# Optimization experiments

Measured on AMD Instinct MI355X. Metric: run time of the kernel, lower is better.

## Reference

```python
import jax, jax.numpy as jnp
import numpy as np

B, H_TRAJ, S = 8, 16, 64
DIM, C = 128, 2000
D = 2 * DIM            # transformer d_model
NUM_HEADS, WINDOW, L = 4, 4, 2
D_FF = 4 * D


def setup_inputs() -> dict:
    key = jax.random.key(0)
    ks = jax.random.split(key, 12)
    w = lambda k, shape, s: jax.random.normal(k, shape, jnp.float32) * s
    return {
        "history": jax.random.randint(ks[0], (B, H_TRAJ, S), 0, C + 1),
        "current_trajectory": jax.random.randint(ks[1], (B, S), 0, C + 1),
        "embedding": w(ks[2], (1, C, DIM), 1.0),
        "null_embedding": jax.random.uniform(ks[3], (D,), jnp.float32),
        "gcn_w": w(ks[4], (DIM, DIM), 0.05),
        "gcn_b": jnp.zeros((DIM,), jnp.float32),
        "enc_attn_w": w(ks[5], (L, 4, D, D), 0.05),
        "enc_attn_b": jnp.zeros((L, 4, D), jnp.float32),
        "enc_ffn_w1": w(ks[6], (L, D, D_FF), 0.05),
        "enc_ffn_b1": jnp.zeros((L, D_FF), jnp.float32),
        "enc_ffn_w2": w(ks[7], (L, D_FF, D), 0.05),
        "enc_ffn_b2": jnp.zeros((L, D), jnp.float32),
        "enc_ln_s": jnp.ones((L, 2, D), jnp.float32),
        "enc_ln_b": jnp.zeros((L, 2, D), jnp.float32),
        "wca_w": w(ks[8], (4, D, D), 0.05),
        "wca_b": jnp.zeros((4, D), jnp.float32),
        "ial_w": w(ks[9], (D, DIM), 0.05),
        "ial_b": jnp.zeros((DIM,), jnp.float32),
    }


def _layer_norm(x, s, b, eps=1e-5):
    m = x.mean(-1, keepdims=True)
    v = ((x - m) ** 2).mean(-1, keepdims=True)
    return (x - m) * jax.lax.rsqrt(v + eps) * s + b


def _mha(xq, xkv, w, b, mask):
    # w: (4,d,d) q/k/v/out, b: (4,d); mask additive, broadcast over heads
    d = xq.shape[-1]
    hd = d // NUM_HEADS
    proj = lambda x, i: (x @ w[i] + b[i]).reshape(x.shape[:-1] + (NUM_HEADS, hd))
    q, k, v = proj(xq, 0), proj(xkv, 1), proj(xkv, 2)
    s = jnp.einsum('bqhd,bkhd->bhqk', q, k) / float(np.sqrt(hd))
    s = s + mask[:, None, :, :]
    a = jax.nn.softmax(s, axis=-1)
    o = jnp.einsum('bhqk,bkhd->bqhd', a, v).reshape(xq.shape)
    return o @ w[3] + b[3]


def _get_graph(history):
    # vectorized scatter-add replacement of the python triple loop
    src, dst = history[:, :, :-1], history[:, :, 1:]
    h_idx = jnp.arange(H_TRAJ, dtype=jnp.float32)
    wts = 1.0 + jnp.exp(-0.01 * (H_TRAJ - 1 - h_idx))          # per-trajectory weight
    valid = (src != C) & (dst != C) & (src != dst)
    wv = jnp.where(valid, wts[None, :, None], 0.0)
    sc, dc = jnp.clip(src, 0, C - 1), jnp.clip(dst, 0, C - 1)
    flat = (jnp.arange(B)[:, None, None] * C * C + sc * C + dc).ravel()
    A = jnp.zeros((B * C * C,), jnp.float32).at[flat].add(wv.ravel())
    return A.reshape(B, C, C)


def _mytransform(A):
    A = A + jnp.eye(C, dtype=A.dtype)
    d = jnp.sqrt(A.sum(axis=1))          # torch code: sqrt of dim-1 sums (no inverse)
    return d[:, :, None] * A * d[:, None, :]   # D @ A @ D


def _temporal(seq_len, d):
    t = jnp.arange(seq_len, dtype=jnp.float32)[:, None]
    den = 10000.0 ** (jnp.arange(0, d, 2, dtype=jnp.float32) / d)
    arg = t / den[None, :]
    return jnp.stack([jnp.sin(arg), jnp.cos(arg)], axis=-1).reshape(seq_len, d)


def _fuse(pos, hist, temp, null_emb):
    # pos: (B,C,D); hist: (B,...,S); gather + where fusion
    g = jax.vmap(lambda p, h: p[h])(pos, jnp.clip(hist, 0, C - 1))
    return jnp.where((hist == C)[..., None], null_emb + temp, g + temp)


def _encoder(x, mask, aw, ab, fw1, fb1, fw2, fb2, lns, lnb):
    for l in range(L):
        a = _mha(x, x, aw[l], ab[l], mask)
        x = _layer_norm(x + a, lns[l, 0], lnb[l, 0])
        f = jax.nn.relu(x @ fw1[l] + fb1[l]) @ fw2[l] + fb2[l]
        x = _layer_norm(x + f, lns[l, 1], lnb[l, 1])
    return x


def reference(history, current_trajectory, embedding, null_embedding, gcn_w, gcn_b,
              enc_attn_w, enc_attn_b, enc_ffn_w1, enc_ffn_b1, enc_ffn_w2, enc_ffn_b2,
              enc_ln_s, enc_ln_b, wca_w, wca_b, ial_w, ial_b):
    E = jnp.broadcast_to(embedding, (B, C, DIM))
    A = _mytransform(_get_graph(history))                      # (B,C,C)
    Eg = jax.nn.relu(A @ E @ gcn_w + gcn_b)                    # GCN layer
    pos = jnp.concatenate([E, Eg], axis=-1)                    # (B,C,2*dim)
    temp = _temporal(S, D)
    fh = _fuse(pos, history, temp, null_embedding).reshape(B * H_TRAJ, S, D)
    fc = _fuse(pos, current_trajectory, temp, null_embedding)  # (B,S,D)
    hmask = jnp.broadcast_to(
        jnp.where((history == C)[:, :, None, :], -jnp.inf, 0.0),
        (B, H_TRAJ, S, S)).reshape(B * H_TRAJ, S, S)
    cmask = jnp.broadcast_to(
        jnp.where((current_trajectory == C)[:, None, :], -jnp.inf, 0.0), (B, S, S))
    mh = _encoder(fh, hmask, enc_attn_w, enc_attn_b, enc_ffn_w1, enc_ffn_b1,
                  enc_ffn_w2, enc_ffn_b2, enc_ln_s, enc_ln_b)
    mc = _encoder(fc, cmask, enc_attn_w, enc_attn_b, enc_ffn_w1, enc_ffn_b1,
                  enc_ffn_w2, enc_ffn_b2, enc_ln_s, enc_ln_b)
    cur_rep = jnp.broadcast_to(mc[:, None], (B, H_TRAJ, S, D)).reshape(B * H_TRAJ, S, D)
    i = jnp.arange(S)
    wmask = jnp.where(jnp.abs(i[:, None] - i[None, :]) <= WINDOW, 0.0, -jnp.inf)[None]
    wca = mh + _mha(mh, cur_rep, wca_w, wca_b, wmask)          # window-based cross attn
    wca = wca.reshape(B, H_TRAJ, S, D)
    # information aggregation over the trajectory axis
    scores = jnp.einsum('bhsd,bsd->bhs', wca, mc) / float(np.sqrt(D))
    aw = jax.nn.softmax(scores, axis=1)
    agg = jnp.einsum('bhs,bhsd->bsd', aw, wca)
    final = jax.nn.relu((agg + mc) @ ial_w + ial_b)            # (B,S,dim)
    return final @ embedding[0].T                              # (B,S,C)
```

## Files before the change

kernel.cpp:

```cpp
#include <hip/hip_runtime.h>
#include <hip/hip_bf16.h>
#include <math.h>

#define C_N   2000
#define DIMN  128
#define DM    256
#define B_N   8
#define HT    16
#define S_N   64
#define NSEQ  136
#define DFF   1024
#define NEDGE (B_N*HT*(S_N-1))

typedef __hip_bfloat16 bf16;
typedef short bf16x8 __attribute__((ext_vector_type(8)));
typedef float f32x4  __attribute__((ext_vector_type(4)));

#define GLOAD_LDS16(gp, lp) \
    __builtin_amdgcn_global_load_lds((const __attribute__((address_space(1))) void*)(gp), \
                                     (__attribute__((address_space(3))) void*)(lp), 16, 0, 0)

__device__ __forceinline__ short f2bf(float v) {
    bf16 t = (bf16)v;
    return *reinterpret_cast<short*>(&t);
}


__global__ void k_initX(const float* __restrict__ cs, const float* __restrict__ Y,
                        const float* __restrict__ gb, float* __restrict__ Eg) {
    size_t i = (size_t)blockIdx.x * 256 + threadIdx.x;
    int k = (int)(i % DIMN); size_t bc = i / DIMN;
    int c = (int)(bc % C_N); int b = (int)(bc / C_N);
    float dd2 = 1.f + cs[b * C_N + c];
    Eg[i] = dd2 * Y[(size_t)c * DIMN + k] + gb[k];
}

__global__ void k_edgeX(const int* __restrict__ hist, const float* __restrict__ cs,
                        const float* __restrict__ Y, float* __restrict__ Eg) {
    int e = blockIdx.x;
    int s = e % (S_N-1); int bh = e / (S_N-1); int h = bh % HT; int b = bh / HT;
    const int* row = hist + (size_t)bh * S_N;
    int src = row[s], dst = row[s+1];
    if (src == C_N || dst == C_N || src == dst) return;
    float w = (1.f + expf(-0.01f * (float)(HT - 1 - h)))
            * sqrtf(1.f + cs[b*C_N+src]) * sqrtf(1.f + cs[b*C_N+dst]);
    int k = threadIdx.x;
    atomicAdd(&Eg[((size_t)b * C_N + src) * DIMN + k], w * Y[(size_t)dst * DIMN + k]);
}

struct TEnt { const float* s; bf16* d; int K; int N; int nm; int tiles; };
struct PrepArgs {
    TEnt e[6];
    const float* emb; bf16* embbf;
    const int* hist; float* colsum;
    float* temp;
};

__global__ void k_prep(PrepArgs p) {
    int id = blockIdx.x;
    int t = threadIdx.y * 32 + threadIdx.x;
    if (id < 1840) {
        __shared__ float tl[32][33];
        TEnt en = p.e[0];
        #pragma unroll
        for (int k = 0; k < 6; ++k) {
            if (id < p.e[k].tiles) { en = p.e[k]; break; }
            id -= p.e[k].tiles;
        }
        int tn = en.N >> 5;
        int per = (en.K >> 5) * tn;
        int mat = id / per, t2 = id % per;
        int ty = t2 / tn, tx = t2 % tn;
        const float* s = en.s + (size_t)mat * en.K * en.N;
        bf16* d = en.d + (size_t)mat * en.N * en.K;
        int k0 = ty * 32, n0 = tx * 32;
        #pragma unroll
        for (int j = 0; j < 32; j += 8)
            tl[threadIdx.y + j][threadIdx.x] = s[(size_t)(k0 + threadIdx.y + j) * en.N + n0 + threadIdx.x];
        __syncthreads();
        #pragma unroll
        for (int j = 0; j < 32; j += 8)
            d[(size_t)(n0 + threadIdx.y + j) * en.K + k0 + threadIdx.x] = (bf16)tl[threadIdx.x][threadIdx.y + j];
        return;
    }
    id -= 1840;
    if (id < 250) {
        int i = (id * 256 + t) * 4;
        float4 v = *(const float4*)(p.emb + i);
        bf16* d = p.embbf;
        d[i] = (bf16)v.x; d[i+1] = (bf16)v.y; d[i+2] = (bf16)v.z; d[i+3] = (bf16)v.w;
        return;
    }
    id -= 250;
    if (id < 32) {
        int e = id * 256 + t;
        if (e >= NEDGE) return;
        int s = e % (S_N-1); int bh = e / (S_N-1); int h = bh % HT; int b = bh / HT;
        const int* row = p.hist + (size_t)bh * S_N;
        int src = row[s], dst = row[s+1];
        if (src != C_N && dst != C_N && src != dst) {
            float w = 1.f + expf(-0.01f * (float)(HT - 1 - h));
            atomicAdd(&p.colsum[b * C_N + dst], w);
        }
        return;
    }
    id -= 32;
    {
        int s = id; int d = t;
        int k = d >> 1;
        float den = powf(10000.f, (2.f * (float)k) / 256.f);
        float arg = (float)s / den;
        p.temp[s * DM + d] = (d & 1) ? cosf(arg) : sinf(arg);
    }
}

template<int EPI>
__global__ __launch_bounds__(256) void k_bgemm(
        const bf16* __restrict__ A, const bf16* __restrict__ Bt,
        const float* __restrict__ bias, const float* __restrict__ resid,
        void* __restrict__ Cout, int M, int N, int K, int ldc, int nreal)
{
    __shared__ bf16 As[2][128 * 64];
    __shared__ bf16 Bs[2][64 * 64];
    int tid = threadIdx.x;
    int wid = tid >> 6, lane = tid & 63;
    int m0 = blockIdx.y * 128, n0 = blockIdx.x * 64;
    int wr = wid >> 1, wc = wid & 1;
    int lr = lane >> 3, lc = lane & 7;
    int gc = lc ^ lr;
    f32x4 acc[4][2] = {};
    int nkt = K >> 6;

#define STAGE_BG(kt, buf) { \
    int kb = (kt) << 6; \
    _Pragma("unroll") \
    for (int s = 0; s < 4; ++s) { \
        int seg = wid * 4 + s; int row = seg * 8 + lr; \
        GLOAD_LDS16(A + (size_t)(m0 + row) * K + kb + gc * 8, &As[buf][seg * 512]); \
    } \
    _Pragma("unroll") \
    for (int s = 0; s < 2; ++s) { \
        int seg = wid * 2 + s; int row = seg * 8 + lr; \
        GLOAD_LDS16(Bt + (size_t)(n0 + row) * K + kb + gc * 8, &Bs[buf][seg * 512]); \
    } }

    STAGE_BG(0, 0);
    __syncthreads();
    int cur = 0;
    for (int kt = 0; kt < nkt; ++kt) {
        if (kt + 1 < nkt) STAGE_BG(kt + 1, cur ^ 1);
        #pragma unroll
        for (int kk = 0; kk < 2; ++kk) {
            bf16x8 af[4], bfr[2];
            int c = kk * 4 + (lane >> 4);
            #pragma unroll
            for (int m = 0; m < 4; ++m) {
                int row = wr * 64 + m * 16 + (lane & 15);
                af[m] = *(const bf16x8*)(&As[cur][row * 64 + (c ^ (row & 7)) * 8]);
            }
            #pragma unroll
            for (int n = 0; n < 2; ++n) {
                int row = wc * 32 + n * 16 + (lane & 15);
                bfr[n] = *(const bf16x8*)(&Bs[cur][row * 64 + (c ^ (row & 7)) * 8]);
            }
            #pragma unroll
            for (int m = 0; m < 4; ++m)
                #pragma unroll
                for (int n = 0; n < 2; ++n)
                    acc[m][n] = __builtin_amdgcn_mfma_f32_16x16x32_bf16(af[m], bfr[n], acc[m][n], 0, 0, 0);
        }
        __syncthreads();
        cur ^= 1;
    }
#undef STAGE_BG
    int cl = lane & 15, ch = lane >> 4;
    #pragma unroll
    for (int n = 0; n < 2; ++n) {
        int col = n0 + wc * 32 + n * 16 + cl;
        if ((EPI & 16) && col >= nreal) continue;
        float bv = (EPI & 1) ? bias[col] : 0.f;
        #pragma unroll
        for (int m = 0; m < 4; ++m) {
            #pragma unroll
            for (int j = 0; j < 4; ++j) {
                int row = m0 + wr * 64 + m * 16 + ch * 4 + j;
                float v = acc[m][n][j] + bv;
                if (EPI & 4) v += resid[(size_t)row * ldc + col];
                if (EPI & 2) v = fmaxf(v, 0.f);
                if (EPI & 8) ((bf16*)Cout)[(size_t)row * ldc + col] = (bf16)v;
                else         ((float*)Cout)[(size_t)row * ldc + col] = v;
            }
        }
    }
}

__global__ __launch_bounds__(256) void k_bgemm_ln(
        const bf16* __restrict__ A, const bf16* __restrict__ Bt,
        const float* __restrict__ bias, float* __restrict__ Xf,
        const float* __restrict__ lns_, const float* __restrict__ lnb_,
        bf16* __restrict__ Xb, int M, int K)
{
    __shared__ bf16 As[2][32 * 64];
    __shared__ bf16 Bs[2][256 * 64];
    __shared__ float ls1[32][4], ls2[32][4];
    int tid = threadIdx.x, wid = tid >> 6, lane = tid & 63;
    int lr = lane >> 3, lc = lane & 7, gc = lc ^ lr;
    int cl = lane & 15, ch = lane >> 4;
    int m0 = blockIdx.x * 32;
    int wc = wid;
    f32x4 acc[2][4] = {};
    int nkt = K >> 6;

#define STAGE_LN(kt, buf) { \
    int kb = (kt) << 6; \
    { int row = wid * 8 + lr; \
      GLOAD_LDS16(A + (size_t)(m0 + row) * K + kb + gc * 8, &As[buf][wid * 512]); } \
    _Pragma("unroll") \
    for (int s = 0; s < 8; ++s) { \
        int seg = wid * 8 + s; int row = seg * 8 + lr; \
        GLOAD_LDS16(Bt + (size_t)row * K + kb + gc * 8, &Bs[buf][seg * 512]); \
    } }

    STAGE_LN(0, 0);
    __syncthreads();
    int cur = 0;
    for (int kt = 0; kt < nkt; ++kt) {
        if (kt + 1 < nkt) STAGE_LN(kt + 1, cur ^ 1);
        #pragma unroll
        for (int kk = 0; kk < 2; ++kk) {
            int c = kk * 4 + ch;
            bf16x8 af[2], bfr[4];
            #pragma unroll
            for (int m = 0; m < 2; ++m) {
                int row = m * 16 + cl;
                af[m] = *(const bf16x8*)(&As[cur][row * 64 + (c ^ (row & 7)) * 8]);
            }
            #pragma unroll
            for (int n = 0; n < 4; ++n) {
                int row = wc * 64 + n * 16 + cl;
                bfr[n] = *(const bf16x8*)(&Bs[cur][row * 64 + (c ^ (row & 7)) * 8]);
            }
            #pragma unroll
            for (int m = 0; m < 2; ++m)
                #pragma unroll
                for (int n = 0; n < 4; ++n)
                    acc[m][n] = __builtin_amdgcn_mfma_f32_16x16x32_bf16(af[m], bfr[n], acc[m][n], 0, 0, 0);
        }
        __syncthreads();
        cur ^= 1;
    }
#undef STAGE_LN
    #pragma unroll
    for (int m = 0; m < 2; ++m) {
        #pragma unroll
        for (int j = 0; j < 4; ++j) {
            int rl = m * 16 + ch * 4 + j;
            float s1 = 0.f, s2 = 0.f;
            #pragma unroll
            for (int n = 0; n < 4; ++n) {
                int col = wc * 64 + n * 16 + cl;
                float v = acc[m][n][j] + bias[col] + Xf[(size_t)(m0 + rl) * 256 + col];
                acc[m][n][j] = v;
                s1 += v; s2 += v * v;
            }
            s1 += __shfl_xor(s1, 1); s2 += __shfl_xor(s2, 1);
            s1 += __shfl_xor(s1, 2); s2 += __shfl_xor(s2, 2);
            s1 += __shfl_xor(s1, 4); s2 += __shfl_xor(s2, 4);
            s1 += __shfl_xor(s1, 8); s2 += __shfl_xor(s2, 8);
            if (cl == 0) { ls1[rl][wc] = s1; ls2[rl][wc] = s2; }
        }
    }
    __syncthreads();
    #pragma unroll
    for (int m = 0; m < 2; ++m) {
        #pragma unroll
        for (int j = 0; j < 4; ++j) {
            int rl = m * 16 + ch * 4 + j;
            float su = ls1[rl][0] + ls1[rl][1] + ls1[rl][2] + ls1[rl][3];
            float sq = ls2[rl][0] + ls2[rl][1] + ls2[rl][2] + ls2[rl][3];
            float mean = su * (1.f / 256.f);
            float var  = sq * (1.f / 256.f) - mean * mean;
            float rstd = rsqrtf(var + 1e-5f);
            #pragma unroll
            for (int n = 0; n < 4; ++n) {
                int col = wc * 64 + n * 16 + cl;
                float r = (acc[m][n][j] - mean) * rstd * lns_[col] + lnb_[col];
                size_t g = (size_t)(m0 + rl) * 256 + col;
                Xf[g] = r;
                Xb[g] = (bf16)r;
            }
        }
    }
}


__global__ void k_fuse(const int* __restrict__ hist, const int* __restrict__ cur,
                       const float* __restrict__ E, const float* __restrict__ Eg,
                       const float* __restrict__ nullE, const float* __restrict__ temp,
                       float* __restrict__ Xenc, bf16* __restrict__ Xbf,
                       float* __restrict__ maskb) {
    int blk = blockIdx.x;
    int seq = blk >> 6, s = blk & 63;
    int d = threadIdx.x;
    int idx, b;
    if (seq < 128) { b = seq >> 4; idx = hist[(size_t)seq * S_N + s]; }
    else           { b = seq - 128; idx = cur[b * S_N + s]; }
    float t = temp[s * DM + d];
    float v;
    if (idx == C_N) v = nullE[d] + t;
    else {
        v = ((d < DIMN) ? E[(size_t)idx * DIMN + d]
                        : fmaxf(Eg[((size_t)b * C_N + idx) * DIMN + (d - DIMN)], 0.f)) + t;
    }
    size_t o = ((size_t)seq * S_N + s) * DM + d;
    Xenc[o] = v;
    Xbf[o]  = (bf16)v;
    if (d == 0) maskb[seq * S_N + s] = (idx == C_N) ? -INFINITY : 0.f;
}

template<bool WCA>
__global__ __launch_bounds__(64) void k_mattn(
        const bf16* __restrict__ Qb, const bf16* __restrict__ Kb,
        const bf16* __restrict__ Vb, const float* __restrict__ maskb,
        bf16* __restrict__ O, int qstr, int kstr)
{
    int seq = blockIdx.x >> 2, head = blockIdx.x & 3;
    int lane = threadIdx.x;
    int cl = lane & 15, ch = lane >> 4;
    __shared__ __align__(16) short VT[64 * 72];
    __shared__ __align__(16) short PT[64 * 72];

    const bf16* Qp = Qb + (size_t)seq * 64 * qstr + head * 64;
    int kvseq = WCA ? (seq >> 4) : seq;
    const bf16* Kp = Kb + (size_t)kvseq * 64 * kstr + head * 64;
    const bf16* Vp = Vb + (size_t)kvseq * 64 * kstr + head * 64;

    bf16x8 aq[4][2], bk[4][2], vr[4][2];
    #pragma unroll
    for (int t = 0; t < 4; ++t)
        #pragma unroll
        for (int kk = 0; kk < 2; ++kk) {
            int row = t * 16 + cl, d0 = kk * 32 + ch * 8;
            aq[t][kk] = *(const bf16x8*)(Qp + (size_t)row * qstr + d0);
            bk[t][kk] = *(const bf16x8*)(Kp + (size_t)row * kstr + d0);
            vr[t][kk] = *(const bf16x8*)(Vp + (size_t)row * kstr + d0);
        }

    f32x4 sa[4][4] = {};
    #pragma unroll
    for (int kk = 0; kk < 2; ++kk)
        #pragma unroll
        for (int m = 0; m < 4; ++m)
            #pragma unroll
            for (int n = 0; n < 4; ++n)
                sa[m][n] = __builtin_amdgcn_mfma_f32_16x16x32_bf16(aq[m][kk], bk[n][kk], sa[m][n], 0, 0, 0);

    #pragma unroll
    for (int t = 0; t < 4; ++t)
        #pragma unroll
        for (int kk = 0; kk < 2; ++kk) {
            int k = t * 16 + cl, d0 = kk * 32 + ch * 8;
            #pragma unroll
            for (int e = 0; e < 8; ++e)
                VT[(d0 + e) * 72 + k] = vr[t][kk][e];
        }

    float mk4[4];
    if (!WCA) {
        #pragma unroll
        for (int n = 0; n < 4; ++n) mk4[n] = maskb[seq * 64 + n * 16 + cl];
    }

    #pragma unroll
    for (int m = 0; m < 4; ++m) {
        #pragma unroll
        for (int j = 0; j < 4; ++j) {
            int q = m * 16 + ch * 4 + j;
            float rm = -INFINITY;
            #pragma unroll
            for (int n = 0; n < 4; ++n) {
                int k = n * 16 + cl;
                float msk = WCA ? ((abs(q - k) <= 4) ? 0.f : -INFINITY) : mk4[n];
                float v = sa[m][n][j] * 0.125f + msk;
                sa[m][n][j] = v;
                rm = fmaxf(rm, v);
            }
            rm = fmaxf(rm, __shfl_xor(rm, 1));
            rm = fmaxf(rm, __shfl_xor(rm, 2));
            rm = fmaxf(rm, __shfl_xor(rm, 4));
            rm = fmaxf(rm, __shfl_xor(rm, 8));
            float rs = 0.f;
            #pragma unroll
            for (int n = 0; n < 4; ++n) {
                float e = expf(sa[m][n][j] - rm);
                sa[m][n][j] = e;
                rs += e;
            }
            rs += __shfl_xor(rs, 1);
            rs += __shfl_xor(rs, 2);
            rs += __shfl_xor(rs, 4);
            rs += __shfl_xor(rs, 8);
            float inv = 1.f / rs;
            #pragma unroll
            for (int n = 0; n < 4; ++n)
                PT[q * 72 + n * 16 + cl] = f2bf(sa[m][n][j] * inv);
        }
    }
    __syncthreads();

    f32x4 oa[4][4] = {};
    #pragma unroll
    for (int kk = 0; kk < 2; ++kk) {
        bf16x8 av[4], bp[4];
        #pragma unroll
        for (int dm = 0; dm < 4; ++dm)
            av[dm] = *(const bf16x8*)(VT + (dm * 16 + cl) * 72 + kk * 32 + ch * 8);
        #pragma unroll
        for (int qn = 0; qn < 4; ++qn)
            bp[qn] = *(const bf16x8*)(PT + (qn * 16 + cl) * 72 + kk * 32 + ch * 8);
        #pragma unroll
        for (int dm = 0; dm < 4; ++dm)
            #pragma unroll
            for (int qn = 0; qn < 4; ++qn)
                oa[dm][qn] = __builtin_amdgcn_mfma_f32_16x16x32_bf16(av[dm], bp[qn], oa[dm][qn], 0, 0, 0);
    }
    __syncthreads();

    #pragma unroll
    for (int dm = 0; dm < 4; ++dm)
        #pragma unroll
        for (int qn = 0; qn < 4; ++qn)
            #pragma unroll
            for (int j = 0; j < 4; ++j)
                PT[(qn * 16 + cl) * 72 + dm * 16 + ch * 4 + j] = f2bf(oa[dm][qn][j]);
    __syncthreads();
    #pragma unroll
    for (int it = 0; it < 8; ++it) {
        int chunk = it * 64 + lane;
        int tok = chunk >> 3, d0 = (chunk & 7) * 8;
        bf16x8 v = *(const bf16x8*)(PT + tok * 72 + d0);
        *(bf16x8*)(O + ((size_t)seq * 64 + tok) * 256 + head * 64 + d0) = v;
    }
}


__global__ __launch_bounds__(256) void k_agg(const float* __restrict__ wca,
                                             const float* __restrict__ mc,
                                             bf16* __restrict__ aggbf) {
    int bs = blockIdx.x; int b = bs >> 6, s = bs & 63;
    int d = threadIdx.x;
    __shared__ float red[4][16];
    float mcv = mc[((size_t)b * S_N + s) * DM + d];
    float wv[16], p[16];
    #pragma unroll
    for (int h = 0; h < 16; ++h) {
        wv[h] = wca[(((size_t)(b * HT + h)) * S_N + s) * DM + d];
        p[h] = wv[h] * mcv;
    }
    #pragma unroll
    for (int o = 1; o < 64; o <<= 1)
        #pragma unroll
        for (int h = 0; h < 16; ++h) p[h] += __shfl_xor(p[h], o);
    if ((d & 63) == 0) {
        int w = d >> 6;
        #pragma unroll
        for (int h = 0; h < 16; ++h) red[w][h] = p[h];
    }
    __syncthreads();
    float sc[16], mx = -INFINITY;
    #pragma unroll
    for (int h = 0; h < 16; ++h) {
        sc[h] = (red[0][h] + red[1][h] + red[2][h] + red[3][h]) * (1.f / 16.f);
        mx = fmaxf(mx, sc[h]);
    }
    float e[16], sum = 0.f;
    #pragma unroll
    for (int h = 0; h < 16; ++h) { e[h] = expf(sc[h] - mx); sum += e[h]; }
    float inv = 1.f / sum;
    float acc = 0.f;
    #pragma unroll
    for (int h = 0; h < 16; ++h) acc += e[h] * inv * wv[h];
    aggbf[((size_t)b * S_N + s) * DM + d] = (bf16)(acc + mcv);
}


extern "C" void kernel_launch(void* const* d_in, const int* in_sizes, int n_in,
                              void* d_out, int out_size, void* d_ws, size_t ws_size,
                              hipStream_t stream) {
    const int*   history = (const int*)d_in[0];
    const int*   cur     = (const int*)d_in[1];
    const float* emb     = (const float*)d_in[2];
    const float* nullE   = (const float*)d_in[3];
    const float* gcn_w   = (const float*)d_in[4];
    const float* gcn_b   = (const float*)d_in[5];
    const float* aw      = (const float*)d_in[6];
    const float* ab      = (const float*)d_in[7];
    const float* fw1     = (const float*)d_in[8];
    const float* fb1     = (const float*)d_in[9];
    const float* fw2     = (const float*)d_in[10];
    const float* fb2     = (const float*)d_in[11];
    const float* lns     = (const float*)d_in[12];
    const float* lnb     = (const float*)d_in[13];
    const float* wca_w   = (const float*)d_in[14];
    const float* wca_b   = (const float*)d_in[15];
    const float* ial_w   = (const float*)d_in[16];
    const float* ial_b   = (const float*)d_in[17];
    float* out = (float*)d_out;
    float* ws  = (float*)d_ws;

    float* dvec   = ws + 0;
    float* maskb  = ws + 16000;
    float* temp   = ws + 24704;
    bf16*  aggbf  = (bf16*)(ws + 41088);
    bf16*  finalb = (bf16*)(ws + 106624);
    bf16*  embbf  = (bf16*)(ws + 139392);
    float* Y      = ws + 270464;
    float* Eg     = ws + 532608;
    bf16*  wbf    = (bf16*)(ws + 2580608);
    float* Xenc   = ws + 3522688;
    bf16*  Xbf    = (bf16*)(ws + 5750912);
    bf16*  Abf    = (bf16*)(ws + 6865024);
    bf16*  Hbf    = (bf16*)(ws + 7979136);
    bf16*  QKVbf  = (bf16*)(ws + 12435584);
    float* SE     = ws + 15777920;

    bf16* wbf_aw  = wbf;
    bf16* wbf_fw1 = wbf + 524288;
    bf16* wbf_fw2 = wbf + 1048576;
    bf16* wbf_wca = wbf + 1572864;
    bf16* wbf_gcn = wbf + 1835008;
    bf16* wbf_ial = wbf + 1851392;

    bf16* Qwbf = QKVbf;
    bf16* KVbf = QKVbf + 4194304;

    hipMemsetAsync(dvec, 0, 16000 * sizeof(float), stream);
    hipMemsetAsync(embbf + 2000 * 128, 0, 48 * 128 * sizeof(bf16), stream);
    PrepArgs pa;
    pa.e[0] = { aw,    wbf_aw,  256,  256, 8, 512 };
    pa.e[1] = { fw1,   wbf_fw1, 256, 1024, 2, 512 };
    pa.e[2] = { fw2,   wbf_fw2, 1024, 256, 2, 512 };
    pa.e[3] = { wca_w, wbf_wca, 256,  256, 4, 256 };
    pa.e[4] = { gcn_w, wbf_gcn, 128,  128, 1,  16 };
    pa.e[5] = { ial_w, wbf_ial, 256,  128, 1,  32 };
    pa.emb = emb; pa.embbf = embbf;
    pa.hist = history; pa.colsum = dvec;
    pa.temp = temp;
    k_prep<<<1840 + 250 + 32 + 64, dim3(32, 8), 0, stream>>>(pa);

    k_bgemm<0><<<dim3(2, 16), 256, 0, stream>>>(embbf, wbf_gcn, nullptr, nullptr, Y,
                                                2048, DIMN, DIMN, DIMN, DIMN);
    k_initX<<<B_N * C_N * DIMN / 256, 256, 0, stream>>>(dvec, Y, gcn_b, Eg);
    k_edgeX<<<NEDGE, 128, 0, stream>>>(history, dvec, Y, Eg);

    k_fuse<<<NSEQ * S_N, DM, 0, stream>>>(history, cur, emb, Eg, nullE, temp, Xenc, Xbf, maskb);

    for (int l = 0; l < 2; ++l) {
        k_bgemm<9><<<dim3(12, 68), 256, 0, stream>>>(Xbf, wbf_aw + l * 262144,
                ab + l * 1024, nullptr, QKVbf, NSEQ * S_N, 768, 256, 768, 768);
        k_mattn<false><<<NSEQ * 4, 64, 0, stream>>>(QKVbf, QKVbf + 256, QKVbf + 512,
                maskb, Abf, 768, 768);
        k_bgemm_ln<<<272, 256, 0, stream>>>(Abf, wbf_aw + l * 262144 + 196608,
                ab + l * 1024 + 768, Xenc, lns + (l * 2 + 0) * DM, lnb + (l * 2 + 0) * DM,
                Xbf, NSEQ * S_N, 256);
        k_bgemm<11><<<dim3(16, 68), 256, 0, stream>>>(Xbf, wbf_fw1 + l * 262144,
                fb1 + l * DFF, nullptr, Hbf, NSEQ * S_N, DFF, 256, DFF, DFF);
        k_bgemm_ln<<<272, 256, 0, stream>>>(Hbf, wbf_fw2 + l * 262144,
                fb2 + l * DM, Xenc, lns + (l * 2 + 1) * DM, lnb + (l * 2 + 1) * DM,
                Xbf, NSEQ * S_N, 1024);
    }

    float* mh = Xenc;
    bf16*  mc_bf = Xbf + (size_t)128 * S_N * DM;

    k_bgemm<9><<<dim3(4, 64), 256, 0, stream>>>(Xbf, wbf_wca, wca_b, nullptr, Qwbf,
                                                128 * S_N, 256, 256, 256, 256);
    k_bgemm<9><<<dim3(8, 4), 256, 0, stream>>>(mc_bf, wbf_wca + 65536, wca_b + 256, nullptr,
                                               KVbf, B_N * S_N, 512, 256, 512, 512);
    k_mattn<true><<<128 * 4, 64, 0, stream>>>(Qwbf, KVbf, KVbf + 256, nullptr, Abf, 256, 512);
    k_bgemm<5><<<dim3(4, 64), 256, 0, stream>>>(Abf, wbf_wca + 196608, wca_b + 768, mh, SE,
                                                128 * S_N, 256, 256, 256, 256);

    k_agg<<<B_N * S_N, 256, 0, stream>>>(SE, Xenc + (size_t)128 * S_N * DM, aggbf);
    k_bgemm<11><<<dim3(2, 4), 256, 0, stream>>>(aggbf, wbf_ial, ial_b, nullptr, finalb,
                                                B_N * S_N, DIMN, DM, DIMN, DIMN);
    k_bgemm<16><<<dim3(32, 4), 256, 0, stream>>>(finalb, embbf, nullptr, nullptr, out,
                                                 B_N * S_N, 2048, DIMN, C_N, C_N);
}
```

Before: 320.7 us.

## Fuse whole pipeline into one cooperative persistent megakernel with grid syncs

```diff
diff --git a/kernel.cpp b/kernel.cpp
--- a/kernel.cpp
+++ b/kernel.cpp
@@ -1,4 +1,5 @@
 #include <hip/hip_runtime.h>
+#include <hip/hip_cooperative_groups.h>
 #include <hip/hip_bf16.h>
 #include <math.h>
 
@@ -16,6 +17,8 @@
 typedef short bf16x8 __attribute__((ext_vector_type(8)));
 typedef float f32x4  __attribute__((ext_vector_type(4)));
 
+namespace cg = cooperative_groups;
+
 #define GLOAD_LDS16(gp, lp) \
     __builtin_amdgcn_global_load_lds((const __attribute__((address_space(1))) void*)(gp), \
                                      (__attribute__((address_space(3))) void*)(lp), 16, 0, 0)
@@ -25,158 +28,98 @@
     return *reinterpret_cast<short*>(&t);
 }
 
-
-__global__ void k_initX(const float* __restrict__ cs, const float* __restrict__ Y,
-                        const float* __restrict__ gb, float* __restrict__ Eg) {
-    size_t i = (size_t)blockIdx.x * 256 + threadIdx.x;
-    int k = (int)(i % DIMN); size_t bc = i / DIMN;
-    int c = (int)(bc % C_N); int b = (int)(bc / C_N);
-    float dd2 = 1.f + cs[b * C_N + c];
-    Eg[i] = dd2 * Y[(size_t)c * DIMN + k] + gb[k];
-}
-
-__global__ void k_edgeX(const int* __restrict__ hist, const float* __restrict__ cs,
-                        const float* __restrict__ Y, float* __restrict__ Eg) {
-    int e = blockIdx.x;
-    int s = e % (S_N-1); int bh = e / (S_N-1); int h = bh % HT; int b = bh / HT;
-    const int* row = hist + (size_t)bh * S_N;
-    int src = row[s], dst = row[s+1];
-    if (src == C_N || dst == C_N || src == dst) return;
-    float w = (1.f + expf(-0.01f * (float)(HT - 1 - h)))
-            * sqrtf(1.f + cs[b*C_N+src]) * sqrtf(1.f + cs[b*C_N+dst]);
-    int k = threadIdx.x;
-    atomicAdd(&Eg[((size_t)b * C_N + src) * DIMN + k], w * Y[(size_t)dst * DIMN + k]);
-}
-
-struct TEnt { const float* s; bf16* d; int K; int N; int nm; int tiles; };
-struct PrepArgs {
-    TEnt e[6];
-    const float* emb; bf16* embbf;
-    const int* hist; float* colsum;
-    float* temp;
+struct MegaArgs {
+    const int *hist, *cur;
+    const float *emb, *nullE, *gcn_b, *ab, *fb1, *fb2, *lns, *lnb, *wca_b, *ial_b;
+    const float *w_aw, *w_fw1, *w_fw2, *w_wca, *w_gcn, *w_ial;
+    float *dvec, *maskb, *temp, *Y, *Eg, *Xenc, *SE, *out;
+    bf16 *embbf, *wbf_aw, *wbf_fw1, *wbf_fw2, *wbf_wca, *wbf_gcn, *wbf_ial;
+    bf16 *Xbf, *Abf, *Hbf, *QKV, *finalb;
 };
 
-__global__ void k_prep(PrepArgs p) {
-    int id = blockIdx.x;
-    int t = threadIdx.y * 32 + threadIdx.x;
-    if (id < 1840) {
-        __shared__ float tl[32][33];
-        TEnt en = p.e[0];
-        #pragma unroll
-        for (int k = 0; k < 6; ++k) {
-            if (id < p.e[k].tiles) { en = p.e[k]; break; }
-            id -= p.e[k].tiles;
-        }
-        int tn = en.N >> 5;
-        int per = (en.K >> 5) * tn;
-        int mat = id / per, t2 = id % per;
-        int ty = t2 / tn, tx = t2 % tn;
-        const float* s = en.s + (size_t)mat * en.K * en.N;
-        bf16* d = en.d + (size_t)mat * en.N * en.K;
-        int k0 = ty * 32, n0 = tx * 32;
-        #pragma unroll
-        for (int j = 0; j < 32; j += 8)
-            tl[threadIdx.y + j][threadIdx.x] = s[(size_t)(k0 + threadIdx.y + j) * en.N + n0 + threadIdx.x];
-        __syncthreads();
-        #pragma unroll
-        for (int j = 0; j < 32; j += 8)
-            d[(size_t)(n0 + threadIdx.y + j) * en.K + k0 + threadIdx.x] = (bf16)tl[threadIdx.x][threadIdx.y + j];
-        return;
-    }
-    id -= 1840;
-    if (id < 250) {
-        int i = (id * 256 + t) * 4;
-        float4 v = *(const float4*)(p.emb + i);
-        bf16* d = p.embbf;
-        d[i] = (bf16)v.x; d[i+1] = (bf16)v.y; d[i+2] = (bf16)v.z; d[i+3] = (bf16)v.w;
-        return;
-    }
-    id -= 250;
-    if (id < 32) {
-        int e = id * 256 + t;
-        if (e >= NEDGE) return;
-        int s = e % (S_N-1); int bh = e / (S_N-1); int h = bh % HT; int b = bh / HT;
-        const int* row = p.hist + (size_t)bh * S_N;
-        int src = row[s], dst = row[s+1];
-        if (src != C_N && dst != C_N && src != dst) {
-            float w = 1.f + expf(-0.01f * (float)(HT - 1 - h));
-            atomicAdd(&p.colsum[b * C_N + dst], w);
-        }
-        return;
-    }
-    id -= 32;
-    {
-        int s = id; int d = t;
-        int k = d >> 1;
-        float den = powf(10000.f, (2.f * (float)k) / 256.f);
-        float arg = (float)s / den;
-        p.temp[s * DM + d] = (d & 1) ? cosf(arg) : sinf(arg);
-    }
+
+__device__ __forceinline__ void transp_unit(const float* __restrict__ src, bf16* __restrict__ dst,
+                                            int K, int N, int tileid, float (*tl)[33]) {
+    int tx = threadIdx.x & 31, ty = (threadIdx.x >> 5) & 7;
+    int tn = N >> 5;
+    int per = (K >> 5) * tn;
+    int mat = tileid / per, t2 = tileid % per;
+    int tyy = t2 / tn, txx = t2 % tn;
+    const float* s = src + (size_t)mat * K * N;
+    bf16* d = dst + (size_t)mat * N * K;
+    int k0 = tyy * 32, n0 = txx * 32;
+    #pragma unroll
+    for (int j = 0; j < 32; j += 8)
+        tl[ty + j][tx] = s[(size_t)(k0 + ty + j) * N + n0 + tx];
+    __syncthreads();
+    #pragma unroll
+    for (int j = 0; j < 32; j += 8)
+        d[(size_t)(n0 + ty + j) * K + k0 + tx] = (bf16)tl[tx][ty + j];
+    __syncthreads();
 }
 
 template<int EPI>
-__global__ __launch_bounds__(256) void k_bgemm(
+__device__ __forceinline__ void bgemm2_tile(
         const bf16* __restrict__ A, const bf16* __restrict__ Bt,
         const float* __restrict__ bias, const float* __restrict__ resid,
-        void* __restrict__ Cout, int M, int N, int K, int ldc, int nreal)
+        void* __restrict__ Cout, int m0, int n0, int K, int ldc, int nreal, char* smemc)
 {
-    __shared__ bf16 As[2][128 * 64];
-    __shared__ bf16 Bs[2][64 * 64];
+    bf16* As = (bf16*)smemc;
+    bf16* Bs = (bf16*)(smemc + 32768);
     int tid = threadIdx.x;
     int wid = tid >> 6, lane = tid & 63;
-    int m0 = blockIdx.y * 128, n0 = blockIdx.x * 64;
     int wr = wid >> 1, wc = wid & 1;
     int lr = lane >> 3, lc = lane & 7;
     int gc = lc ^ lr;
-    f32x4 acc[4][2] = {};
+    f32x4 acc[4][4] = {};
     int nkt = K >> 6;
 
-#define STAGE_BG(kt, buf) { \
+#define STAGE2(kt, buf) { \
     int kb = (kt) << 6; \
     _Pragma("unroll") \
     for (int s = 0; s < 4; ++s) { \
         int seg = wid * 4 + s; int row = seg * 8 + lr; \
-        GLOAD_LDS16(A + (size_t)(m0 + row) * K + kb + gc * 8, &As[buf][seg * 512]); \
+        GLOAD_LDS16(A + (size_t)(m0 + row) * K + kb + gc * 8, As + (buf) * 8192 + seg * 512); \
     } \
     _Pragma("unroll") \
-    for (int s = 0; s < 2; ++s) { \
-        int seg = wid * 2 + s; int row = seg * 8 + lr; \
-        GLOAD_LDS16(Bt + (size_t)(n0 + row) * K + kb + gc * 8, &Bs[buf][seg * 512]); \
+    for (int s = 0; s < 4; ++s) { \
+        int seg = wid * 4 + s; int row = seg * 8 + lr; \
+        GLOAD_LDS16(Bt + (size_t)(n0 + row) * K + kb + gc * 8, Bs + (buf) * 8192 + seg * 512); \
     } }
 
-    STAGE_BG(0, 0);
+    STAGE2(0, 0);
     __syncthreads();
     int cur = 0;
     for (int kt = 0; kt < nkt; ++kt) {
-        if (kt + 1 < nkt) STAGE_BG(kt + 1, cur ^ 1);
+        if (kt + 1 < nkt) STAGE2(kt + 1, cur ^ 1);
         #pragma unroll
         for (int kk = 0; kk < 2; ++kk) {
-            bf16x8 af[4], bfr[2];
+            bf16x8 af[4], bfr[4];
             int c = kk * 4 + (lane >> 4);
             #pragma unroll
             for (int m = 0; m < 4; ++m) {
                 int row = wr * 64 + m * 16 + (lane & 15);
-                af[m] = *(const bf16x8*)(&As[cur][row * 64 + (c ^ (row & 7)) * 8]);
-            }
-            #pragma unroll
-            for (int n = 0; n < 2; ++n) {
-                int row = wc * 32 + n * 16 + (lane & 15);
-                bfr[n] = *(const bf16x8*)(&Bs[cur][row * 64 + (c ^ (row & 7)) * 8]);
+                af[m] = *(const bf16x8*)(As + cur * 8192 + row * 64 + (c ^ (row & 7)) * 8);
+            }
+            #pragma unroll
+            for (int n = 0; n < 4; ++n) {
+                int row = wc * 64 + n * 16 + (lane & 15);
+                bfr[n] = *(const bf16x8*)(Bs + cur * 8192 + row * 64 + (c ^ (row & 7)) * 8);
             }
             #pragma unroll
             for (int m = 0; m < 4; ++m)
                 #pragma unroll
-                for (int n = 0; n < 2; ++n)
+                for (int n = 0; n < 4; ++n)
                     acc[m][n] = __builtin_amdgcn_mfma_f32_16x16x32_bf16(af[m], bfr[n], acc[m][n], 0, 0, 0);
         }
         __syncthreads();
         cur ^= 1;
     }
-#undef STAGE_BG
+#undef STAGE2
     int cl = lane & 15, ch = lane >> 4;
     #pragma unroll
-    for (int n = 0; n < 2; ++n) {
-        int col = n0 + wc * 32 + n * 16 + cl;
+    for (int n = 0; n < 4; ++n) {
+        int col = n0 + wc * 64 + n * 16 + cl;
         if ((EPI & 16) && col >= nreal) continue;
         float bv = (EPI & 1) ? bias[col] : 0.f;
         #pragma unroll
@@ -194,19 +137,19 @@
     }
 }
 
-__global__ __launch_bounds__(256) void k_bgemm_ln(
+__device__ __forceinline__ void bgemm_ln_tile(
         const bf16* __restrict__ A, const bf16* __restrict__ Bt,
         const float* __restrict__ bias, float* __restrict__ Xf,
         const float* __restrict__ lns_, const float* __restrict__ lnb_,
-        bf16* __restrict__ Xb, int M, int K)
+        bf16* __restrict__ Xb, int m0, int K, char* smemc)
 {
-    __shared__ bf16 As[2][32 * 64];
-    __shared__ bf16 Bs[2][256 * 64];
-    __shared__ float ls1[32][4], ls2[32][4];
+    bf16* As  = (bf16*)smemc;
+    bf16* Bs  = (bf16*)(smemc + 8192);
+    float* ls1 = (float*)(smemc + 73728);
+    float* ls2 = ls1 + 128;
     int tid = threadIdx.x, wid = tid >> 6, lane = tid & 63;
     int lr = lane >> 3, lc = lane & 7, gc = lc ^ lr;
     int cl = lane & 15, ch = lane >> 4;
-    int m0 = blockIdx.x * 32;
     int wc = wid;
     f32x4 acc[2][4] = {};
     int nkt = K >> 6;
@@ -214,11 +157,11 @@
 #define STAGE_LN(kt, buf) { \
     int kb = (kt) << 6; \
     { int row = wid * 8 + lr; \
-      GLOAD_LDS16(A + (size_t)(m0 + row) * K + kb + gc * 8, &As[buf][wid * 512]); } \
+      GLOAD_LDS16(A + (size_t)(m0 + row) * K + kb + gc * 8, As + (buf) * 2048 + wid * 512); } \
     _Pragma("unroll") \
     for (int s = 0; s < 8; ++s) { \
         int seg = wid * 8 + s; int row = seg * 8 + lr; \
-        GLOAD_LDS16(Bt + (size_t)row * K + kb + gc * 8, &Bs[buf][seg * 512]); \
+        GLOAD_LDS16(Bt + (size_t)row * K + kb + gc * 8, Bs + (buf) * 16384 + seg * 512); \
     } }
 
     STAGE_LN(0, 0);
@@ -233,12 +176,12 @@
             #pragma unroll
             for (int m = 0; m < 2; ++m) {
                 int row = m * 16 + cl;
-                af[m] = *(const bf16x8*)(&As[cur][row * 64 + (c ^ (row & 7)) * 8]);
+                af[m] = *(const bf16x8*)(As + cur * 2048 + row * 64 + (c ^ (row & 7)) * 8);
             }
             #pragma unroll
             for (int n = 0; n < 4; ++n) {
                 int row = wc * 64 + n * 16 + cl;
-                bfr[n] = *(const bf16x8*)(&Bs[cur][row * 64 + (c ^ (row & 7)) * 8]);
+                bfr[n] = *(const bf16x8*)(Bs + cur * 16384 + row * 64 + (c ^ (row & 7)) * 8);
             }
             #pragma unroll
             for (int m = 0; m < 2; ++m)
@@ -267,7 +210,7 @@
             s1 += __shfl_xor(s1, 2); s2 += __shfl_xor(s2, 2);
             s1 += __shfl_xor(s1, 4); s2 += __shfl_xor(s2, 4);
             s1 += __shfl_xor(s1, 8); s2 += __shfl_xor(s2, 8);
-            if (cl == 0) { ls1[rl][wc] = s1; ls2[rl][wc] = s2; }
+            if (cl == 0) { ls1[rl * 4 + wc] = s1; ls2[rl * 4 + wc] = s2; }
         }
     }
     __syncthreads();
@@ -276,8 +219,8 @@
         #pragma unroll
         for (int j = 0; j < 4; ++j) {
             int rl = m * 16 + ch * 4 + j;
-            float su = ls1[rl][0] + ls1[rl][1] + ls1[rl][2] + ls1[rl][3];
-            float sq = ls2[rl][0] + ls2[rl][1] + ls2[rl][2] + ls2[rl][3];
+            float su = ls1[rl*4+0] + ls1[rl*4+1] + ls1[rl*4+2] + ls1[rl*4+3];
+            float sq = ls2[rl*4+0] + ls2[rl*4+1] + ls2[rl*4+2] + ls2[rl*4+3];
             float mean = su * (1.f / 256.f);
             float var  = sq * (1.f / 256.f) - mean * mean;
             float rstd = rsqrtf(var + 1e-5f);
@@ -291,45 +234,18 @@
             }
         }
     }
-}
-
-
-__global__ void k_fuse(const int* __restrict__ hist, const int* __restrict__ cur,
-                       const float* __restrict__ E, const float* __restrict__ Eg,
-                       const float* __restrict__ nullE, const float* __restrict__ temp,
-                       float* __restrict__ Xenc, bf16* __restrict__ Xbf,
-                       float* __restrict__ maskb) {
-    int blk = blockIdx.x;
-    int seq = blk >> 6, s = blk & 63;
-    int d = threadIdx.x;
-    int idx, b;
-    if (seq < 128) { b = seq >> 4; idx = hist[(size_t)seq * S_N + s]; }
-    else           { b = seq - 128; idx = cur[b * S_N + s]; }
-    float t = temp[s * DM + d];
-    float v;
-    if (idx == C_N) v = nullE[d] + t;
-    else {
-        v = ((d < DIMN) ? E[(size_t)idx * DIMN + d]
-                        : fmaxf(Eg[((size_t)b * C_N + idx) * DIMN + (d - DIMN)], 0.f)) + t;
-    }
-    size_t o = ((size_t)seq * S_N + s) * DM + d;
-    Xenc[o] = v;
-    Xbf[o]  = (bf16)v;
-    if (d == 0) maskb[seq * S_N + s] = (idx == C_N) ? -INFINITY : 0.f;
+    __syncthreads();
 }
 
 template<bool WCA>
-__global__ __launch_bounds__(64) void k_mattn(
-        const bf16* __restrict__ Qb, const bf16* __restrict__ Kb,
+__device__ __forceinline__ void mattn_unit(
+        int seq, int head, const bf16* __restrict__ Qb, const bf16* __restrict__ Kb,
         const bf16* __restrict__ Vb, const float* __restrict__ maskb,
-        bf16* __restrict__ O, int qstr, int kstr)
+        bf16* __restrict__ O, short* VT, short* PT, int lane)
 {
-    int seq = blockIdx.x >> 2, head = blockIdx.x & 3;
-    int lane = threadIdx.x;
+    const int qstr = WCA ? 256 : 768;
+    const int kstr = WCA ? 512 : 768;
     int cl = lane & 15, ch = lane >> 4;
-    __shared__ __align__(16) short VT[64 * 72];
-    __shared__ __align__(16) short PT[64 * 72];
-
     const bf16* Qp = Qb + (size_t)seq * 64 * qstr + head * 64;
     int kvseq = WCA ? (seq >> 4) : seq;
     const bf16* Kp = Kb + (size_t)kvseq * 64 * kstr + head * 64;
@@ -345,7 +261,6 @@
             bk[t][kk] = *(const bf16x8*)(Kp + (size_t)row * kstr + d0);
             vr[t][kk] = *(const bf16x8*)(Vp + (size_t)row * kstr + d0);
         }
-
     f32x4 sa[4][4] = {};
     #pragma unroll
     for (int kk = 0; kk < 2; ++kk)
@@ -354,7 +269,6 @@
             #pragma unroll
             for (int n = 0; n < 4; ++n)
                 sa[m][n] = __builtin_amdgcn_mfma_f32_16x16x32_bf16(aq[m][kk], bk[n][kk], sa[m][n], 0, 0, 0);
-
     #pragma unroll
     for (int t = 0; t < 4; ++t)
         #pragma unroll
@@ -364,13 +278,11 @@
             for (int e = 0; e < 8; ++e)
                 VT[(d0 + e) * 72 + k] = vr[t][kk][e];
         }
-
     float mk4[4];
     if (!WCA) {
         #pragma unroll
         for (int n = 0; n < 4; ++n) mk4[n] = maskb[seq * 64 + n * 16 + cl];
     }
-
     #pragma unroll
     for (int m = 0; m < 4; ++m) {
         #pragma unroll
@@ -407,7 +319,6 @@
         }
     }
     __syncthreads();
-
     f32x4 oa[4][4] = {};
     #pragma unroll
     for (int kk = 0; kk < 2; ++kk) {
@@ -425,7 +336,6 @@
                 oa[dm][qn] = __builtin_amdgcn_mfma_f32_16x16x32_bf16(av[dm], bp[qn], oa[dm][qn], 0, 0, 0);
     }
     __syncthreads();
-
     #pragma unroll
     for (int dm = 0; dm < 4; ++dm)
         #pragma unroll
@@ -443,18 +353,70 @@
     }
 }
 
-
-__global__ __launch_bounds__(256) void k_agg(const float* __restrict__ wca,
-                                             const float* __restrict__ mc,
-                                             bf16* __restrict__ aggbf) {
-    int bs = blockIdx.x; int b = bs >> 6, s = bs & 63;
+__device__ __forceinline__ void fuse_unit(const MegaArgs& a, int u, int d) {
+    int seq = u >> 6, s = u & 63;
+    int idx, b;
+    if (seq < 128) { b = seq >> 4; idx = a.hist[(size_t)seq * S_N + s]; }
+    else           { b = seq - 128; idx = a.cur[b * S_N + s]; }
+    float t = a.temp[s * DM + d];
+    float v;
+    if (idx == C_N) v = a.nullE[d] + t;
+    else {
+        v = ((d < DIMN) ? a.emb[(size_t)idx * DIMN + d]
+                        : fmaxf(a.Eg[((size_t)b * C_N + idx) * DIMN + (d - DIMN)], 0.f)) + t;
+    }
+    size_t o = (size_t)u * DM + d;
+    a.Xenc[o] = v;
+    a.Xbf[o]  = (bf16)v;
+    if (d == 0) a.maskb[u] = (idx == C_N) ? -INFINITY : 0.f;
+}
+
+__device__ __forceinline__ void initx_unit(const MegaArgs& a, int u, int tid) {
+    int i0 = u * 1024 + tid * 4;
+    int k = i0 & 127; int bc = i0 >> 7; int c = bc % C_N; int b = bc / C_N;
+    float dd2 = 1.f + a.dvec[b * C_N + c];
+    float4 y = *(const float4*)(a.Y + (size_t)c * DIMN + k);
+    float4 o = { dd2 * y.x + a.gcn_b[k],     dd2 * y.y + a.gcn_b[k + 1],
+                 dd2 * y.z + a.gcn_b[k + 2], dd2 * y.w + a.gcn_b[k + 3] };
+    *(float4*)(a.Eg + i0) = o;
+}
+
+__device__ __forceinline__ void edge_unit(const MegaArgs& a, int u, int tid) {
+    int e = u * 2 + (tid >> 7); int k = tid & 127;
+    int s = e % (S_N-1); int bh = e / (S_N-1); int h = bh % HT; int b = bh / HT;
+    const int* row = a.hist + (size_t)bh * S_N;
+    int src = row[s], dst = row[s+1];
+    if (src == C_N || dst == C_N || src == dst) return;
+    float w = (1.f + expf(-0.01f * (float)(HT - 1 - h)))
+            * sqrtf(1.f + a.dvec[b*C_N+src]) * sqrtf(1.f + a.dvec[b*C_N+dst]);
+    atomicAdd(&a.Eg[((size_t)b * C_N + src) * DIMN + k], w * a.Y[(size_t)dst * DIMN + k]);
+}
+
+__device__ __forceinline__ void colsum_unit(const MegaArgs& a, int u, int tid) {
+    int e = u * 256 + tid;
+    if (e >= NEDGE) return;
+    int s = e % (S_N-1); int bh = e / (S_N-1); int h = bh % HT; int b = bh / HT;
+    const int* row = a.hist + (size_t)bh * S_N;
+    int src = row[s], dst = row[s+1];
+    if (src != C_N && dst != C_N && src != dst) {
+        float w = 1.f + expf(-0.01f * (float)(HT - 1 - h));
+        atomicAdd(&a.dvec[b * C_N + dst], w);
+    }
+}
+
+__device__ __forceinline__ void agg_ial_unit(int u, const float* __restrict__ SE,
+        const float* __restrict__ mc, const bf16* __restrict__ ialw,
+        const float* __restrict__ ialb, bf16* __restrict__ finalb, char* smemc)
+{
+    float* red  = (float*)smemc;
+    float* aggs = (float*)(smemc + 256);
+    int b = u >> 6, s = u & 63;
     int d = threadIdx.x;
-    __shared__ float red[4][16];
     float mcv = mc[((size_t)b * S_N + s) * DM + d];
     float wv[16], p[16];
     #pragma unroll
     for (int h = 0; h < 16; ++h) {
-        wv[h] = wca[(((size_t)(b * HT + h)) * S_N + s) * DM + d];
+        wv[h] = SE[(((size_t)(b * HT + h)) * S_N + s) * DM + d];
         p[h] = wv[h] * mcv;
     }
     #pragma unroll
@@ -464,13 +426,13 @@
     if ((d & 63) == 0) {
         int w = d >> 6;
         #pragma unroll
-        for (int h = 0; h < 16; ++h) red[w][h] = p[h];
+        for (int h = 0; h < 16; ++h) red[w * 16 + h] = p[h];
     }
     __syncthreads();
     float sc[16], mx = -INFINITY;
     #pragma unroll
     for (int h = 0; h < 16; ++h) {
-        sc[h] = (red[0][h] + red[1][h] + red[2][h] + red[3][h]) * (1.f / 16.f);
+        sc[h] = (red[h] + red[16 + h] + red[32 + h] + red[48 + h]) * (1.f / 16.f);
         mx = fmaxf(mx, sc[h]);
     }
     float e[16], sum = 0.f;
@@ -480,38 +442,184 @@
     float acc = 0.f;
     #pragma unroll
     for (int h = 0; h < 16; ++h) acc += e[h] * inv * wv[h];
-    aggbf[((size_t)b * S_N + s) * DM + d] = (bf16)(acc + mcv);
+    aggs[d] = acc + mcv;
+    __syncthreads();
+    if (d < 128) {
+        float sumo = ialb[d];
+        #pragma unroll 8
+        for (int k = 0; k < 256; ++k) sumo += aggs[k] * (float)ialw[d * 256 + k];
+        finalb[(size_t)u * 128 + d] = (bf16)fmaxf(sumo, 0.f);
+    }
+    __syncthreads();
+}
+
+__device__ __forceinline__ void prep_unit(const MegaArgs& a, int u, int tid, char* smemc) {
+    if (u < 1840) {
+        const float* s; bf16* d; int K, N, t0;
+        if      (u < 512)  { s = a.w_aw;  d = a.wbf_aw;  K = 256;  N = 256;  t0 = u; }
+        else if (u < 1024) { s = a.w_fw1; d = a.wbf_fw1; K = 256;  N = 1024; t0 = u - 512; }
+        else if (u < 1536) { s = a.w_fw2; d = a.wbf_fw2; K = 1024; N = 256;  t0 = u - 1024; }
+        else if (u < 1792) { s = a.w_wca; d = a.wbf_wca; K = 256;  N = 256;  t0 = u - 1536; }
+        else if (u < 1808) { s = a.w_gcn; d = a.wbf_gcn; K = 128;  N = 128;  t0 = u - 1792; }
+        else               { s = a.w_ial; d = a.wbf_ial; K = 256;  N = 128;  t0 = u - 1808; }
+        transp_unit(s, d, K, N, t0, (float(*)[33])smemc);
+    } else if (u < 2090) {
+        int i = ((u - 1840) * 256 + tid) * 4;
+        float4 v = *(const float4*)(a.emb + i);
+        a.embbf[i] = (bf16)v.x; a.embbf[i+1] = (bf16)v.y;
+        a.embbf[i+2] = (bf16)v.z; a.embbf[i+3] = (bf16)v.w;
+    } else if (u < 2154) {
+        int s = u - 2090; int d = tid;
+        int k = d >> 1;
+        float den = powf(10000.f, (2.f * (float)k) / 256.f);
+        float arg = (float)s / den;
+        a.temp[s * DM + d] = (d & 1) ? cosf(arg) : sinf(arg);
+    } else if (u < 2170) {
+        int i4 = (u - 2154) * 256 + tid;
+        if (i4 < 4000) { float4 z = {0,0,0,0}; *(float4*)(a.dvec + i4 * 4) = z; }
+    } else {
+        int* p = (int*)(a.embbf + 2000 * 128);
+        for (int j = tid; j < 3072; j += 256) p[j] = 0;
+    }
+}
+
+
+__global__ __launch_bounds__(256, 2) void k_mega(MegaArgs a) {
+    cg::grid_group grid = cg::this_grid();
+    __shared__ __align__(16) char smem[74752];
+    const int nb = gridDim.x, bid = blockIdx.x;
+    const int tid = threadIdx.x, wid = tid >> 6, lane = tid & 63;
+
+    for (int u = bid; u < 2171; u += nb) prep_unit(a, u, tid, smem);
+    grid.sync();
+    for (int u = bid; u < 48; u += nb) {
+        if (u < 16) bgemm2_tile<0>(a.embbf, a.wbf_gcn, nullptr, nullptr, a.Y,
+                                   u * 128, 0, 128, 128, 0, smem);
+        else colsum_unit(a, u - 16, tid);
+    }
+    grid.sync();
+    for (int u = bid; u < 2000; u += nb) initx_unit(a, u, tid);
+    grid.sync();
+    for (int u = bid; u < 4032; u += nb) edge_unit(a, u, tid);
+    grid.sync();
+    for (int u = bid; u < 8704; u += nb) fuse_unit(a, u, tid);
+    grid.sync();
+    for (int l = 0; l < 2; ++l) {
+        const bf16* wqkv = a.wbf_aw + l * 262144;
+        const float* bl = a.ab + l * 1024;
+        for (int u = bid; u < 408; u += nb)
+            bgemm2_tile<9>(a.Xbf, wqkv, bl, nullptr, a.QKV,
+                           (u / 6) * 128, (u % 6) * 128, 256, 768, 0, smem);
+        grid.sync();
+        for (int u = bid; u < 136; u += nb)
+            mattn_unit<false>(u, wid, a.QKV, a.QKV + 256, a.QKV + 512, a.maskb, a.Abf,
+                              (short*)(smem + wid * 18432), (short*)(smem + wid * 18432 + 9216), lane);
+        grid.sync();
+        for (int u = bid; u < 272; u += nb)
+            bgemm_ln_tile(a.Abf, wqkv + 196608, bl + 768, a.Xenc,
+                          a.lns + (l * 2) * DM, a.lnb + (l * 2) * DM, a.Xbf, u * 32, 256, smem);
+        grid.sync();
+        for (int u = bid; u < 544; u += nb)
+            bgemm2_tile<11>(a.Xbf, a.wbf_fw1 + l * 262144, a.fb1 + l * DFF, nullptr, a.Hbf,
+                            (u / 8) * 128, (u % 8) * 128, 256, DFF, 0, smem);
+        grid.sync();
+        for (int u = bid; u < 272; u += nb)
+            bgemm_ln_tile(a.Hbf, a.wbf_fw2 + l * 262144, a.fb2 + l * DM, a.Xenc,
+                          a.lns + (l * 2 + 1) * DM, a.lnb + (l * 2 + 1) * DM, a.Xbf, u * 32, 1024, smem);
+        grid.sync();
+    }
+    for (int u = bid; u < 144; u += nb) {
+        if (u < 128)
+            bgemm2_tile<9>(a.Xbf, a.wbf_wca, a.wca_b, nullptr, a.QKV,
+                           (u >> 1) * 128, (u & 1) * 128, 256, 256, 0, smem);
+        else {
+            int v = u - 128;
+            bgemm2_tile<9>(a.Xbf + (size_t)128 * S_N * DM, a.wbf_wca + 65536, a.wca_b + 256,
+                           nullptr, a.QKV + 4194304, (v >> 2) * 128, (v & 3) * 128, 256, 512, 0, smem);
+        }
+    }
+    grid.sync();
+    for (int u = bid; u < 128; u += nb)
+        mattn_unit<true>(u, wid, a.QKV, a.QKV + 4194304, a.QKV + 4194304 + 256, nullptr, a.Abf,
+                         (short*)(smem + wid * 18432), (short*)(smem + wid * 18432 + 9216), lane);
+    grid.sync();
+    for (int u = bid; u < 128; u += nb)
+        bgemm2_tile<5>(a.Abf, a.wbf_wca + 196608, a.wca_b + 768, a.Xenc, a.SE,
+                       (u >> 1) * 128, (u & 1) * 128, 256, 256, 0, smem);
+    grid.sync();
+    for (int u = bid; u < 512; u += nb)
+        agg_ial_unit(u, a.SE, a.Xenc + (size_t)128 * S_N * DM, a.wbf_ial, a.ial_b, a.finalb, smem);
+    grid.sync();
+    for (int u = bid; u < 64; u += nb)
+        bgemm2_tile<16>(a.finalb, a.embbf, nullptr, nullptr, a.out,
+                        (u >> 4) * 128, (u & 15) * 128, 128, C_N, C_N, smem);
+}
+
+
+__global__ void k_prepg(MegaArgs a) {
+    __shared__ __align__(16) char sm[4352];
+    int id = blockIdx.x, tid = threadIdx.x;
+    if (id < 1840) { prep_unit(a, id, tid, sm); return; }
+    id -= 1840;
+    if (id < 250) { prep_unit(a, 1840 + id, tid, sm); return; }
+    id -= 250;
+    if (id < 32) { colsum_unit(a, id, tid); return; }
+    id -= 32;
+    prep_unit(a, 2090 + id, tid, sm);
+}
+
+__global__ void k_initXg(MegaArgs a) { initx_unit(a, blockIdx.x, threadIdx.x); }
+__global__ void k_edgeXg(MegaArgs a) { edge_unit(a, blockIdx.x, threadIdx.x); }
+__global__ void k_fuseg(MegaArgs a)  { fuse_unit(a, blockIdx.x, threadIdx.x); }
+
+template<int EPI>
+__global__ __launch_bounds__(256) void k_bgemm2g(
+        const bf16* A, const bf16* Bt, const float* bias, const float* resid,
+        void* C, int K, int ldc, int nreal) {
+    __shared__ __align__(16) char sm[65536];
+    bgemm2_tile<EPI>(A, Bt, bias, resid, C, blockIdx.y * 128, blockIdx.x * 128, K, ldc, nreal, sm);
+}
+
+__global__ __launch_bounds__(256) void k_wcaqkvg(
+        const bf16* Xbf, const bf16* mcbf, const bf16* w, const float* wb,
+        bf16* Q, bf16* KV) {
+    __shared__ __align__(16) char sm[65536];
+    int u = blockIdx.x;
+    if (u < 128) bgemm2_tile<9>(Xbf, w, wb, nullptr, Q, (u >> 1) * 128, (u & 1) * 128, 256, 256, 0, sm);
+    else { int v = u - 128;
+           bgemm2_tile<9>(mcbf, w + 65536, wb + 256, nullptr, KV, (v >> 2) * 128, (v & 3) * 128, 256, 512, 0, sm); }
+}
+
+__global__ __launch_bounds__(256) void k_bgemm_lng(
+        const bf16* A, const bf16* Bt, const float* bias, float* Xf,
+        const float* lns_, const float* lnb_, bf16* Xb, int K) {
+    __shared__ __align__(16) char sm[74752];
+    bgemm_ln_tile(A, Bt, bias, Xf, lns_, lnb_, Xb, blockIdx.x * 32, K, sm);
+}
+
+template<bool WCA>
+__global__ __launch_bounds__(64) void k_mattng(
+        const bf16* Qb, const bf16* Kb, const bf16* Vb, const float* maskb, bf16* O) {
+    __shared__ __align__(16) char sm[18432];
+    mattn_unit<WCA>(blockIdx.x >> 2, blockIdx.x & 3, Qb, Kb, Vb, maskb, O,
+                    (short*)sm, (short*)(sm + 9216), threadIdx.x);
+}
+
+__global__ __launch_bounds__(256) void k_aggialg(
+        const float* SE, const float* mc, const bf16* ialw, const float* ialb, bf16* finalb) {
+    __shared__ __align__(16) char sm[2048];
+    agg_ial_unit(blockIdx.x, SE, mc, ialw, ialb, finalb, sm);
 }
 
 
 extern "C" void kernel_launch(void* const* d_in, const int* in_sizes, int n_in,
                               void* d_out, int out_size, void* d_ws, size_t ws_size,
                               hipStream_t stream) {
-    const int*   history = (const int*)d_in[0];
-    const int*   cur     = (const int*)d_in[1];
-    const float* emb     = (const float*)d_in[2];
-    const float* nullE   = (const float*)d_in[3];
-    const float* gcn_w   = (const float*)d_in[4];
-    const float* gcn_b   = (const float*)d_in[5];
-    const float* aw      = (const float*)d_in[6];
-    const float* ab      = (const float*)d_in[7];
-    const float* fw1     = (const float*)d_in[8];
-    const float* fb1     = (const float*)d_in[9];
-    const float* fw2     = (const float*)d_in[10];
-    const float* fb2     = (const float*)d_in[11];
-    const float* lns     = (const float*)d_in[12];
-    const float* lnb     = (const float*)d_in[13];
-    const float* wca_w   = (const float*)d_in[14];
-    const float* wca_b   = (const float*)d_in[15];
-    const float* ial_w   = (const float*)d_in[16];
-    const float* ial_b   = (const float*)d_in[17];
-    float* out = (float*)d_out;
-    float* ws  = (float*)d_ws;
+    float* ws = (float*)d_ws;
 
     float* dvec   = ws + 0;
     float* maskb  = ws + 16000;
     float* temp   = ws + 24704;
-    bf16*  aggbf  = (bf16*)(ws + 41088);
     bf16*  finalb = (bf16*)(ws + 106624);
     bf16*  embbf  = (bf16*)(ws + 139392);
     float* Y      = ws + 270464;
@@ -519,71 +627,67 @@
     bf16*  wbf    = (bf16*)(ws + 2580608);
     float* Xenc   = ws + 3522688;
     bf16*  Xbf    = (bf16*)(ws + 5750912);
-    bf16*  Abf    = (bf16*)(ws + 6865024);
-    bf16*  Hbf    = (bf16*)(ws + 7979136);
-    bf16*  QKVbf  = (bf16*)(ws + 12435584);
-    float* SE     = ws + 15777920;
-
-    bf16* wbf_aw  = wbf;
-    bf16* wbf_fw1 = wbf + 524288;
-    bf16* wbf_fw2 = wbf + 1048576;
-    bf16* wbf_wca = wbf + 1572864;
-    bf16* wbf_gcn = wbf + 1835008;
-    bf16* wbf_ial = wbf + 1851392;
-
-    bf16* Qwbf = QKVbf;
-    bf16* KVbf = QKVbf + 4194304;
+    bf16*  Hbf    = (bf16*)(ws + 6865024);
+    bf16*  QKVbf  = (bf16*)(ws + 11321472);
+    float* SE     = ws + 14663808;
+
+    MegaArgs a;
+    a.hist  = (const int*)d_in[0];   a.cur   = (const int*)d_in[1];
+    a.emb   = (const float*)d_in[2]; a.nullE = (const float*)d_in[3];
+    a.w_gcn = (const float*)d_in[4]; a.gcn_b = (const float*)d_in[5];
+    a.w_aw  = (const float*)d_in[6]; a.ab    = (const float*)d_in[7];
+    a.w_fw1 = (const float*)d_in[8]; a.fb1   = (const float*)d_in[9];
+    a.w_fw2 = (const float*)d_in[10]; a.fb2  = (const float*)d_in[11];
+    a.lns   = (const float*)d_in[12]; a.lnb  = (const float*)d_in[13];
+    a.w_wca = (const float*)d_in[14]; a.wca_b = (const float*)d_in[15];
+    a.w_ial = (const float*)d_in[16]; a.ial_b = (const float*)d_in[17];
+    a.dvec = dvec; a.maskb = maskb; a.temp = temp; a.Y = Y; a.Eg = Eg;
+    a.Xenc = Xenc; a.SE = SE; a.out = (float*)d_out;
+    a.embbf = embbf;
+    a.wbf_aw = wbf; a.wbf_fw1 = wbf + 524288; a.wbf_fw2 = wbf + 1048576;
+    a.wbf_wca = wbf + 1572864; a.wbf_gcn = wbf + 1835008; a.wbf_ial = wbf + 1851392;
+    a.Xbf = Xbf; a.Abf = Hbf; a.Hbf = Hbf; a.QKV = QKVbf; a.finalb = finalb;
+
+    hipError_t st = hipErrorNotSupported;
+    int dev = 0; hipGetDevice(&dev);
+    int coop = 0; hipDeviceGetAttribute(&coop, hipDeviceAttributeCooperativeLaunch, dev);
+    if (coop) {
+        int occ = 0;
+        hipOccupancyMaxActiveBlocksPerMultiprocessor(&occ, (const void*)k_mega, 256, 0);
+        int nblk = (occ > 0 ? occ : 1) * 256;
+        if (nblk > 512) nblk = 512;
+        void* params[] = { (void*)&a };
+        st = hipLaunchCooperativeKernel((const void*)k_mega, dim3(nblk), dim3(256),
+                                        params, 0, stream);
+    }
+    if (st == hipSuccess) return;
 
     hipMemsetAsync(dvec, 0, 16000 * sizeof(float), stream);
     hipMemsetAsync(embbf + 2000 * 128, 0, 48 * 128 * sizeof(bf16), stream);
-    PrepArgs pa;
-    pa.e[0] = { aw,    wbf_aw,  256,  256, 8, 512 };
-    pa.e[1] = { fw1,   wbf_fw1, 256, 1024, 2, 512 };
-    pa.e[2] = { fw2,   wbf_fw2, 1024, 256, 2, 512 };
-    pa.e[3] = { wca_w, wbf_wca, 256,  256, 4, 256 };
-    pa.e[4] = { gcn_w, wbf_gcn, 128,  128, 1,  16 };
-    pa.e[5] = { ial_w, wbf_ial, 256,  128, 1,  32 };
-    pa.emb = emb; pa.embbf = embbf;
-    pa.hist = history; pa.colsum = dvec;
-    pa.temp = temp;
-    k_prep<<<1840 + 250 + 32 + 64, dim3(32, 8), 0, stream>>>(pa);
-
-    k_bgemm<0><<<dim3(2, 16), 256, 0, stream>>>(embbf, wbf_gcn, nullptr, nullptr, Y,
-                                                2048, DIMN, DIMN, DIMN, DIMN);
-    k_initX<<<B_N * C_N * DIMN / 256, 256, 0, stream>>>(dvec, Y, gcn_b, Eg);
-    k_edgeX<<<NEDGE, 128, 0, stream>>>(history, dvec, Y, Eg);
-
-    k_fuse<<<NSEQ * S_N, DM, 0, stream>>>(history, cur, emb, Eg, nullE, temp, Xenc, Xbf, maskb);
-
+    k_prepg<<<2186, 256, 0, stream>>>(a);
+    k_bgemm2g<0><<<dim3(1, 16), 256, 0, stream>>>(embbf, a.wbf_gcn, nullptr, nullptr, Y, 128, 128, 0);
+    k_initXg<<<2000, 256, 0, stream>>>(a);
+    k_edgeXg<<<4032, 256, 0, stream>>>(a);
+    k_fuseg<<<8704, 256, 0, stream>>>(a);
     for (int l = 0; l < 2; ++l) {
-        k_bgemm<9><<<dim3(12, 68), 256, 0, stream>>>(Xbf, wbf_aw + l * 262144,
-                ab + l * 1024, nullptr, QKVbf, NSEQ * S_N, 768, 256, 768, 768);
-        k_mattn<false><<<NSEQ * 4, 64, 0, stream>>>(QKVbf, QKVbf + 256, QKVbf + 512,
-                maskb, Abf, 768, 768);
-        k_bgemm_ln<<<272, 256, 0, stream>>>(Abf, wbf_aw + l * 262144 + 196608,
-                ab + l * 1024 + 768, Xenc, lns + (l * 2 + 0) * DM, lnb + (l * 2 + 0) * DM,
-                Xbf, NSEQ * S_N, 256);
-        k_bgemm<11><<<dim3(16, 68), 256, 0, stream>>>(Xbf, wbf_fw1 + l * 262144,
-                fb1 + l * DFF, nullptr, Hbf, NSEQ * S_N, DFF, 256, DFF, DFF);
-        k_bgemm_ln<<<272, 256, 0, stream>>>(Hbf, wbf_fw2 + l * 262144,
-                fb2 + l * DM, Xenc, lns + (l * 2 + 1) * DM, lnb + (l * 2 + 1) * DM,
-                Xbf, NSEQ * S_N, 1024);
-    }
-
-    float* mh = Xenc;
-    bf16*  mc_bf = Xbf + (size_t)128 * S_N * DM;
-
-    k_bgemm<9><<<dim3(4, 64), 256, 0, stream>>>(Xbf, wbf_wca, wca_b, nullptr, Qwbf,
-                                                128 * S_N, 256, 256, 256, 256);
-    k_bgemm<9><<<dim3(8, 4), 256, 0, stream>>>(mc_bf, wbf_wca + 65536, wca_b + 256, nullptr,
-                                               KVbf, B_N * S_N, 512, 256, 512, 512);
-    k_mattn<true><<<128 * 4, 64, 0, stream>>>(Qwbf, KVbf, KVbf + 256, nullptr, Abf, 256, 512);
-    k_bgemm<5><<<dim3(4, 64), 256, 0, stream>>>(Abf, wbf_wca + 196608, wca_b + 768, mh, SE,
-                                                128 * S_N, 256, 256, 256, 256);
-
-    k_agg<<<B_N * S_N, 256, 0, stream>>>(SE, Xenc + (size_t)128 * S_N * DM, aggbf);
-    k_bgemm<11><<<dim3(2, 4), 256, 0, stream>>>(aggbf, wbf_ial, ial_b, nullptr, finalb,
-                                                B_N * S_N, DIMN, DM, DIMN, DIMN);
-    k_bgemm<16><<<dim3(32, 4), 256, 0, stream>>>(finalb, embbf, nullptr, nullptr, out,
-                                                 B_N * S_N, 2048, DIMN, C_N, C_N);
-}
+        const bf16* wqkv = a.wbf_aw + l * 262144;
+        const float* bl = a.ab + l * 1024;
+        k_bgemm2g<9><<<dim3(6, 68), 256, 0, stream>>>(Xbf, wqkv, bl, nullptr, QKVbf, 256, 768, 0);
+        k_mattng<false><<<544, 64, 0, stream>>>(QKVbf, QKVbf + 256, QKVbf + 512, maskb, a.Abf);
+        k_bgemm_lng<<<272, 256, 0, stream>>>(a.Abf, wqkv + 196608, bl + 768, Xenc,
+                a.lns + (l * 2) * DM, a.lnb + (l * 2) * DM, Xbf, 256);
+        k_bgemm2g<11><<<dim3(8, 68), 256, 0, stream>>>(Xbf, a.wbf_fw1 + l * 262144,
+                a.fb1 + l * DFF, nullptr, Hbf, 256, DFF, 0);
+        k_bgemm_lng<<<272, 256, 0, stream>>>(Hbf, a.wbf_fw2 + l * 262144, a.fb2 + l * DM, Xenc,
+                a.lns + (l * 2 + 1) * DM, a.lnb + (l * 2 + 1) * DM, Xbf, 1024);
+    }
+    bf16* mc_bf = Xbf + (size_t)128 * S_N * DM;
+    k_wcaqkvg<<<144, 256, 0, stream>>>(Xbf, mc_bf, a.wbf_wca, a.wca_b, QKVbf, QKVbf + 4194304);
+    k_mattng<true><<<512, 64, 0, stream>>>(QKVbf, QKVbf + 4194304, QKVbf + 4194304 + 256,
+                                           nullptr, a.Abf);
+    k_bgemm2g<5><<<dim3(2, 64), 256, 0, stream>>>(a.Abf, a.wbf_wca + 196608, a.wca_b + 768,
+                                                  Xenc, SE, 256, 256, 0);
+    k_aggialg<<<512, 256, 0, stream>>>(SE, Xenc + (size_t)128 * S_N * DM, a.wbf_ial, a.ial_b, finalb);
+    k_bgemm2g<16><<<dim3(16, 4), 256, 0, stream>>>(finalb, embbf, nullptr, nullptr,
+                                                   (float*)d_out, 128, C_N, C_N);
+}
```

New measurement: 1.038 ms. 224% more time.
